# Kernel optimization log

Measured on AMD Instinct MI355X. Metric: run time of the kernel, lower is better.

Reference implementation:

```python
import jax, jax.numpy as jnp
import numpy as np

LAMDA = 0.2  # config['lamda']
T, B, NI, IL, NS, H = 24, 64, 32, 24, 256, 256  # steps, batch, n_inputs, input_len(=vec), n_stations, hidden


def setup_inputs() -> dict:
    key = jax.random.key(0)
    ks = jax.random.split(key, 24)
    VEC, DIN = IL, NI + NS
    n = lambda k, s, sc=1.0: jax.random.normal(k, s, dtype=jnp.float32) * sc
    return {
        'local_inputs': n(ks[0], (T, B, NI)),
        'global_inputs': n(ks[1], (T, B, NS)),
        'local_states': n(ks[2], (B, NI, IL)),
        'global_states': n(ks[3], (B, NS, NI, IL)),
        'distmat': n(ks[4], (B, NS)),
        'local_attn0': jax.random.uniform(ks[5], (B, NI), jnp.float32, -0.25, 0.25),
        'global_attn0': jax.random.uniform(ks[6], (B, NS), jnp.float32, -0.15, 0.15),
        # conv_local_u: 1x1 conv over [B, IL, NI, 1] -> weight [VEC, IL]
        'Wcl': n(ks[7], (VEC, IL), 0.1), 'bcl': n(ks[8], (VEC,), 0.05),
        'Wll': n(ks[9], (VEC, H), 0.05), 'bll': n(ks[10], (VEC,), 0.05),
        'vl': n(ks[11], (VEC,)),
        # conv_global_k: kernel (1, NI) over [B, IL, NS, NI] -> weight [VEC, IL, NI]
        'Wcg': n(ks[12], (VEC, IL, NI), 0.05), 'bcg': n(ks[13], (VEC,), 0.05),
        'Wlg': n(ks[14], (VEC, H), 0.05), 'blg': n(ks[15], (VEC,), 0.05),
        'vg': n(ks[16], (VEC,)),
        # LSTM cell (called with zero h0/c0 every step, as in the source)
        'Wih': n(ks[17], (4 * H, DIN), 0.05),
        'bih': n(ks[18], (4 * H,), 0.05),
        'bhh': n(ks[19], (4 * H,), 0.05),
    }


def reference(local_inputs, global_inputs, local_states, global_states, distmat,
              local_attn0, global_attn0, Wcl, bcl, Wll, bll, vl,
              Wcg, bcg, Wlg, blg, vg, Wih, bih, bhh):
    b, ni, il = local_states.shape
    ns = global_states.shape[1]
    # raw .view() reshapes as in the torch code (NOT transposes)
    lhid = local_states.reshape(b, il, ni)                 # [B, IL, NI]
    hf_l = jnp.einsum('oc,bcl->bol', Wcl, lhid) + bcl[None, :, None]   # 1x1 conv
    ghid = global_states.reshape(b, il, ns, ni)            # [B, IL, NS, NI]
    hf_g = jnp.einsum('ocj,bcsj->bos', Wcg, ghid) + bcg[None, :, None]  # (1,NI) conv

    def step(carry, xs):
        la, ga = carry
        l_inp, g_inp = xs
        x = jnp.concatenate([la * l_inp, ga * g_inp], axis=1)  # [B, NI+NS]
        gates = x @ Wih.T + bih + bhh                          # h0 = 0 -> no Whh term
        i_g, f_g, g_g, o_g = jnp.split(gates, 4, axis=1)       # torch gate order i,f,g,o
        c = jax.nn.sigmoid(i_g) * jnp.tanh(g_g)                # c0 = 0 -> forget term drops
        h = jax.nn.sigmoid(o_g) * jnp.tanh(c)
        q = c                                                  # query = LSTM state
        y_l = q @ Wll.T + bll                                  # [B, VEC]
        s_l = jnp.einsum('bold,d->bl', jnp.tanh(hf_l[:, :, :, None] + y_l[:, None, None, :]), vl)
        la_n = jax.nn.softmax(s_l, axis=1)
        y_g = q @ Wlg.T + blg
        s_g = jnp.einsum('bosd,d->bs', jnp.tanh(hf_g[:, :, :, None] + y_g[:, None, None, :]), vg)
        s_g = (1.0 - LAMDA) * s_g + LAMDA * distmat
        ga_n = jax.nn.softmax(s_g, axis=1)
        return (la_n, ga_n), (h, c, la_n, ga_n)

    _, (outs, cs, las, gas) = jax.lax.scan(step, (local_attn0, global_attn0),
                                           (local_inputs, global_inputs))
    return outs, cs[-1], las, gas
```

## Files before the change

kernel.cpp:

```cpp
#include <hip/hip_runtime.h>

#define T_     24
#define LAMDA_ 0.2f

#define OFF_CS  393216
#define OFF_LAS 409600
#define OFF_GAS 458752

__device__ __forceinline__ float clamp15(float x){ return fminf(15.f, fmaxf(-15.f, x)); }
__device__ __forceinline__ float rcp_(float x){ return __builtin_amdgcn_rcpf(x); }

__global__ __launch_bounds__(1024, 4) void spat_kernel(
    const float* __restrict__ li,  const float* __restrict__ gi,
    const float* __restrict__ ls,  const float* __restrict__ gs,
    const float* __restrict__ dist,
    const float* __restrict__ la0, const float* __restrict__ ga0,
    const float* __restrict__ Wcl, const float* __restrict__ bcl,
    const float* __restrict__ Wll, const float* __restrict__ bll, const float* __restrict__ vl,
    const float* __restrict__ Wcg, const float* __restrict__ bcg,
    const float* __restrict__ Wlg, const float* __restrict__ blg, const float* __restrict__ vg,
    const float* __restrict__ Wih, const float* __restrict__ bih, const float* __restrict__ bhh,
    float* __restrict__ out)
{
    __shared__ float Eg[6144];
    __shared__ float El[800];
    __shared__ float outb[6144];
    __shared__ float gasb[6144];
    __shared__ float lasb[768];
    __shared__ float csb[256];
    __shared__ __align__(16) union {
        float wcg[6144];
        struct {
            float sgred[1024];
            float gbuf[768];
            float xv[288];
            float cq[256];
            float slg[32];
        } p;
    } U;
    __shared__ float dstf[256];
    __shared__ float bsum[768];
    __shared__ float bcf[48];
    __shared__ __align__(16) float4 pl4[12], pg4[12];
    __shared__ float vlf[24], vgf[24], cbuf[2];

    const int b = blockIdx.x, tid = threadIdx.x;
    const int s = tid & 255, ogrp = tid >> 8;

    if (tid < 256) dstf[tid] = dist[b*256 + tid];
    if (tid < 24)  { vlf[tid] = vl[tid]; vgf[tid] = vg[tid]; }
    if (tid < 48)  bcf[tid] = (tid < 24) ? bll[tid] : blg[tid - 24];
    if (tid < 768) {
        const int wrow = tid + ((tid >= 256) ? 256 : 0);
        bsum[tid] = bih[wrow] + bhh[wrow];
    }
    if (tid == 0)  { float s1 = 0.f; for (int d = 0; d < 24; d++) s1 += vl[d]; cbuf[0] = s1; }
    if (tid == 1)  { float s1 = 0.f; for (int d = 0; d < 24; d++) s1 += vg[d]; cbuf[1] = s1; }

    float acc[6];
#pragma unroll
    for (int i = 0; i < 6; i++) acc[i] = bcg[ogrp*6 + i];

    for (int hc = 0; hc < 3; hc++) {
        for (int k = tid; k < 6144; k += 1024) {
            const int o = k >> 8, r = k & 255;
            U.wcg[k] = Wcg[o*768 + hc*256 + r];
        }
        __syncthreads();
        for (int cc = 0; cc < 8; cc++) {
            const int c = hc*8 + cc;
            const float4* gp = (const float4*)(gs + ((size_t)b*196608 + c*8192 + s*32));
#pragma unroll
            for (int h = 0; h < 2; h++) {
                float gv[16];
#pragma unroll
                for (int m = 0; m < 4; m++) {
                    const float4 g = gp[h*4 + m];
                    gv[4*m] = g.x; gv[4*m+1] = g.y; gv[4*m+2] = g.z; gv[4*m+3] = g.w;
                }
#pragma unroll
                for (int i = 0; i < 6; i++) {
                    const float4* wp = (const float4*)(U.wcg + ((ogrp*6 + i)*256 + cc*32)) + h*4;
                    float a = acc[i];
#pragma unroll
                    for (int m = 0; m < 4; m++) {
                        const float4 w = wp[m];
                        a = fmaf(w.x, gv[4*m],   a);
                        a = fmaf(w.y, gv[4*m+1], a);
                        a = fmaf(w.z, gv[4*m+2], a);
                        a = fmaf(w.w, gv[4*m+3], a);
                    }
                    acc[i] = a;
                }
            }
        }
        __syncthreads();
    }
#pragma unroll
    for (int i = 0; i < 6; i++) Eg[(ogrp*6 + i)*256 + s] = __expf(2.f*clamp15(acc[i]));

    if (tid < 768) {
        const int o = tid >> 5, l = tid & 31;
        float a = bcl[o];
        for (int c = 0; c < 24; c++)
            a = fmaf(Wcl[o*24 + c], ls[b*768 + c*32 + l], a);
        El[l*25 + o] = __expf(2.f*clamp15(a));
    }

    if (tid < 288) {
        if (tid < 32) U.p.xv[tid] = la0[b*32 + tid] * li[b*32 + tid];
        else { const int ss = tid - 32; U.p.xv[tid] = ga0[b*256 + ss] * gi[b*256 + ss]; }
    }
    __syncthreads();

    const int u8 = tid & 7, slot = tid >> 3;
    const int rbase = slot*6;
    const int lg = tid >> 5, ol = tid & 31;

    for (int t = 0; t < T_; t++) {
        float liN = 0.f;
        float giN0 = 0.f, giN1 = 0.f, giN2 = 0.f, giN3 = 0.f;
        if (t < T_ - 1) {
            if (tid < 32) liN = li[(t+1)*2048 + b*32 + tid];
            else if (tid >= 64 && tid < 128) {
                const int lane = tid - 64;
                giN0 = gi[(t+1)*16384 + b*256 + lane];
                giN1 = gi[(t+1)*16384 + b*256 + lane + 64];
                giN2 = gi[(t+1)*16384 + b*256 + lane + 128];
                giN3 = gi[(t+1)*16384 + b*256 + lane + 192];
            }
        }

        {
            const float4* xp = (const float4*)U.p.xv;
            float ar0 = 0.f, ar1 = 0.f, ar2 = 0.f, ar3 = 0.f, ar4 = 0.f, ar5 = 0.f;
#pragma unroll 1
            for (int jc = 0; jc < 3; jc++) {
                const float4 x0 = xp[jc*24 + u8];
                const float4 x1 = xp[jc*24 + 8 + u8];
                const float4 x2 = xp[jc*24 + 16 + u8];

#define KROW(kk, AR) { \
                const int row_ = rbase + (kk); \
                const int wrow_ = row_ + ((row_ >= 256) ? 256 : 0); \
                const float4* wp_ = (const float4*)(Wih + wrow_*288) + jc*24 + u8; \
                const float4 w0_ = wp_[0], w1_ = wp_[8], w2_ = wp_[16]; \
                float a_ = AR; \
                a_ = fmaf(w0_.x,x0.x,a_); a_ = fmaf(w0_.y,x0.y,a_); \
                a_ = fmaf(w0_.z,x0.z,a_); a_ = fmaf(w0_.w,x0.w,a_); \
                a_ = fmaf(w1_.x,x1.x,a_); a_ = fmaf(w1_.y,x1.y,a_); \
                a_ = fmaf(w1_.z,x1.z,a_); a_ = fmaf(w1_.w,x1.w,a_); \
                a_ = fmaf(w2_.x,x2.x,a_); a_ = fmaf(w2_.y,x2.y,a_); \
                a_ = fmaf(w2_.z,x2.z,a_); a_ = fmaf(w2_.w,x2.w,a_); \
                AR = a_; }

                KROW(0, ar0) KROW(1, ar1) KROW(2, ar2)
                __builtin_amdgcn_sched_barrier(0);
                KROW(3, ar3) KROW(4, ar4) KROW(5, ar5)
                __builtin_amdgcn_sched_barrier(0);
#undef KROW
            }
            {
                float a_;
#define RED(kk, AR) { a_ = AR; \
                a_ += __shfl_xor(a_, 1); a_ += __shfl_xor(a_, 2); a_ += __shfl_xor(a_, 4); \
                if (u8 == 0) { const int row_ = rbase + (kk); U.p.gbuf[row_] = a_ + bsum[row_]; } }
                RED(0, ar0) RED(1, ar1) RED(2, ar2) RED(3, ar3) RED(4, ar4) RED(5, ar5)
#undef RED
            }
        }
        __syncthreads();

        if (tid < 256) {
            const float ig = U.p.gbuf[tid], gg = U.p.gbuf[256 + tid], ot = U.p.gbuf[512 + tid];
            const float sig_i = rcp_(1.f + __expf(-ig));
            const float th_g  = 1.f - 2.f*rcp_(1.f + __expf(2.f*clamp15(gg)));
            const float c     = sig_i * th_g;
            const float sig_o = rcp_(1.f + __expf(-ot));
            const float th_c  = 1.f - 2.f*rcp_(1.f + __expf(2.f*c));
            const float h     = sig_o * th_c;
            U.p.cq[tid] = c;
            outb[t*256 + tid] = h;
            if (t == T_ - 1) csb[tid] = c;
        }
        __syncthreads();

        if (tid < 384) {
            const int dot = slot;
            const float* Wr = (dot < 24) ? (Wll + dot*256) : (Wlg + (dot - 24)*256);
            const float4* wp = (const float4*)Wr;
            const float4* cp = (const float4*)U.p.cq;
            float a0 = 0.f, a1 = 0.f;
#pragma unroll
            for (int j = 0; j < 8; j += 2) {
                const float4 w0 = wp[j*8 + u8],     c0 = cp[j*8 + u8];
                const float4 w1 = wp[(j+1)*8 + u8], c1 = cp[(j+1)*8 + u8];
                a0 = fmaf(w0.x,c0.x,a0); a0 = fmaf(w0.y,c0.y,a0);
                a0 = fmaf(w0.z,c0.z,a0); a0 = fmaf(w0.w,c0.w,a0);
                a1 = fmaf(w1.x,c1.x,a1); a1 = fmaf(w1.y,c1.y,a1);
                a1 = fmaf(w1.z,c1.z,a1); a1 = fmaf(w1.w,c1.w,a1);
            }
            float a = a0 + a1;
            a += __shfl_xor(a, 1); a += __shfl_xor(a, 2); a += __shfl_xor(a, 4);
            const float F  = __expf(2.f*clamp15(a + bcf[dot]));
            const float v  = (dot < 24) ? vlf[dot] : vgf[dot - 24];
            const float Fo = __shfl_xor(F, 8);
            const float vo = (dot < 24) ? vlf[dot ^ 1] : vgf[(dot ^ 1) - 24];
            if ((tid & 15) == 0) {
                const float A0 = v + vo;
                const float A1 = fmaf(v, Fo, vo * F);
                const float B1 = F + Fo;
                const float B2 = F * Fo;
                const int P = slot >> 1;
                if (P < 12) pl4[P]      = make_float4(A0, A1, B1, B2);
                else        pg4[P - 12] = make_float4(A0, A1, B1, B2);
            }
        }
        __syncthreads();

        {
            float z[6], z2[6];
#pragma unroll
            for (int i = 0; i < 6; i++) {
                z[i]  = Eg[(ogrp*6 + i)*256 + s];
                z2[i] = z[i]*z[i];
            }
            float a0 = 0.f;
#pragma unroll 4
            for (int p = 0; p < 12; p++) {
                const float4 q = pg4[p];
#pragma unroll
                for (int i = 0; i < 6; i++) {
                    const float num = fmaf(z[i],  q.y, q.x);
                    const float den = fmaf(z2[i], q.w, fmaf(z[i], q.z, 1.f));
                    a0 = fmaf(num, rcp_(den), a0);
                }
            }
            U.p.sgred[tid] = a0;
        }
        {
            float bsl = 0.f;
            if (ol < 24) {
                const float E  = El[lg*25 + ol];
                const float E2 = E*E;
#pragma unroll 4
                for (int p = 0; p < 12; p++) {
                    const float4 q = pl4[p];
                    const float num = fmaf(E,  q.y, q.x);
                    const float den = fmaf(E2, q.w, fmaf(E, q.z, 1.f));
                    bsl = fmaf(num, rcp_(den), bsl);
                }
            }
            bsl += __shfl_xor(bsl, 1);  bsl += __shfl_xor(bsl, 2);
            bsl += __shfl_xor(bsl, 4);  bsl += __shfl_xor(bsl, 8);
            bsl += __shfl_xor(bsl, 16);
            if (ol == 0) U.p.slg[lg] = bsl;
        }
        __syncthreads();

        if (tid < 32) {
            const float sv = 24.f*cbuf[0] - 2.f*U.p.slg[tid];
            float m = sv;
#pragma unroll
            for (int mk = 16; mk >= 1; mk >>= 1) m = fmaxf(m, __shfl_xor(m, mk));
            const float e = __expf(sv - m);
            float ss = e;
#pragma unroll
            for (int mk = 16; mk >= 1; mk >>= 1) ss += __shfl_xor(ss, mk);
            const float r = e * rcp_(ss);
            lasb[t*32 + tid] = r;
            if (t < T_ - 1) U.p.xv[tid] = r * liN;
        } else if (tid >= 64 && tid < 128) {
            const int lane = tid - 64;
            float vv0, vv1, vv2, vv3;
            {
                const float t0 = U.p.sgred[lane]     + U.p.sgred[256+lane]     + U.p.sgred[512+lane]     + U.p.sgred[768+lane];
                const float t1 = U.p.sgred[lane+64]  + U.p.sgred[256+lane+64]  + U.p.sgred[512+lane+64]  + U.p.sgred[768+lane+64];
                const float t2 = U.p.sgred[lane+128] + U.p.sgred[256+lane+128] + U.p.sgred[512+lane+128] + U.p.sgred[768+lane+128];
                const float t3 = U.p.sgred[lane+192] + U.p.sgred[256+lane+192] + U.p.sgred[512+lane+192] + U.p.sgred[768+lane+192];
                vv0 = (1.f-LAMDA_)*(24.f*cbuf[1] - 2.f*t0) + LAMDA_*dstf[lane];
                vv1 = (1.f-LAMDA_)*(24.f*cbuf[1] - 2.f*t1) + LAMDA_*dstf[lane+64];
                vv2 = (1.f-LAMDA_)*(24.f*cbuf[1] - 2.f*t2) + LAMDA_*dstf[lane+128];
                vv3 = (1.f-LAMDA_)*(24.f*cbuf[1] - 2.f*t3) + LAMDA_*dstf[lane+192];
            }
            float m = fmaxf(fmaxf(vv0, vv1), fmaxf(vv2, vv3));
#pragma unroll
            for (int mk = 32; mk >= 1; mk >>= 1) m = fmaxf(m, __shfl_xor(m, mk));
            const float e0 = __expf(vv0 - m), e1 = __expf(vv1 - m);
            const float e2 = __expf(vv2 - m), e3 = __expf(vv3 - m);
            float ss = (e0 + e1) + (e2 + e3);
#pragma unroll
            for (int mk = 32; mk >= 1; mk >>= 1) ss += __shfl_xor(ss, mk);
            const float inv = rcp_(ss);
            const float r0 = e0*inv, r1 = e1*inv, r2 = e2*inv, r3 = e3*inv;
            float* gb = gasb + t*256;
            gb[lane] = r0; gb[lane+64] = r1; gb[lane+128] = r2; gb[lane+192] = r3;
            if (t < T_ - 1) {
                U.p.xv[32+lane]     = r0 * giN0;
                U.p.xv[32+lane+64]  = r1 * giN1;
                U.p.xv[32+lane+128] = r2 * giN2;
                U.p.xv[32+lane+192] = r3 * giN3;
            }
        }
        __syncthreads();
    }

    for (int k = tid; k < 6144; k += 1024) {
        const int tt = k >> 8, ii = k & 255;
        out[tt*16384 + b*256 + ii]           = outb[k];
        out[OFF_GAS + tt*16384 + b*256 + ii] = gasb[k];
    }
    if (tid < 768) out[OFF_LAS + (tid >> 5)*2048 + b*32 + (tid & 31)] = lasb[tid];
    if (tid < 256) out[OFF_CS + b*256 + tid] = csb[tid];
}

extern "C" void kernel_launch(void* const* d_in, const int* in_sizes, int n_in,
                              void* d_out, int out_size, void* d_ws, size_t ws_size,
                              hipStream_t stream)
{
    const float* li   = (const float*)d_in[0];
    const float* gi   = (const float*)d_in[1];
    const float* ls   = (const float*)d_in[2];
    const float* gs   = (const float*)d_in[3];
    const float* dist = (const float*)d_in[4];
    const float* la0  = (const float*)d_in[5];
    const float* ga0  = (const float*)d_in[6];
    const float* Wcl  = (const float*)d_in[7];
    const float* bcl  = (const float*)d_in[8];
    const float* Wll  = (const float*)d_in[9];
    const float* bll  = (const float*)d_in[10];
    const float* vl   = (const float*)d_in[11];
    const float* Wcg  = (const float*)d_in[12];
    const float* bcg  = (const float*)d_in[13];
    const float* Wlg  = (const float*)d_in[14];
    const float* blg  = (const float*)d_in[15];
    const float* vg   = (const float*)d_in[16];
    const float* Wih  = (const float*)d_in[17];
    const float* bih  = (const float*)d_in[18];
    const float* bhh  = (const float*)d_in[19];

    spat_kernel<<<64, 1024, 0, stream>>>(li, gi, ls, gs, dist, la0, ga0,
                                         Wcl, bcl, Wll, bll, vl,
                                         Wcg, bcg, Wlg, blg, vg,
                                         Wih, bih, bhh, (float*)d_out);
}
```

Baseline: 506.2 us.

## Replace per-element tanh attention sums with per-step cubic-interpolated lookup tables

Result: slower. 535.0 us (+5.7%).

```diff
diff --git a/kernel.cpp b/kernel.cpp
--- a/kernel.cpp
+++ b/kernel.cpp
@@ -6,6 +6,10 @@
 #define OFF_CS  393216
 #define OFF_LAS 409600
 #define OFF_GAS 458752
+
+#define TBL_N   1024
+#define TBL_H   (32.0f/1023.0f)
+#define TBL_IH  (1023.0f/32.0f)
 
 __device__ __forceinline__ float clamp15(float x){ return fminf(15.f, fmaxf(-15.f, x)); }
 __device__ __forceinline__ float rcp_(float x){ return __builtin_amdgcn_rcpf(x); }
@@ -22,8 +26,6 @@
     const float* __restrict__ Wih, const float* __restrict__ bih, const float* __restrict__ bhh,
     float* __restrict__ out)
 {
-    __shared__ float Eg[6144];
-    __shared__ float El[800];
     __shared__ float outb[6144];
     __shared__ float gasb[6144];
     __shared__ float lasb[768];
@@ -38,10 +40,12 @@
             float slg[32];
         } p;
     } U;
+    __shared__ float gt[TBL_N];
+    __shared__ float lt[TBL_N];
+    __shared__ __align__(8) float2 ygp[24], ylp[24];
     __shared__ float dstf[256];
     __shared__ float bsum[768];
     __shared__ float bcf[48];
-    __shared__ __align__(16) float4 pl4[12], pg4[12];
     __shared__ float vlf[24], vgf[24], cbuf[2];
 
     const int b = blockIdx.x, tid = threadIdx.x;
@@ -96,15 +100,34 @@
         }
         __syncthreads();
     }
-#pragma unroll
-    for (int i = 0; i < 6; i++) Eg[(ogrp*6 + i)*256 + s] = __expf(2.f*clamp15(acc[i]));
-
-    if (tid < 768) {
-        const int o = tid >> 5, l = tid & 31;
-        float a = bcl[o];
+
+    const int lg = tid >> 5, ol = tid & 31;
+
+    float al_a = 0.f;
+    if (ol < 24) {
+        float a = bcl[ol];
         for (int c = 0; c < 24; c++)
-            a = fmaf(Wcl[o*24 + c], ls[b*768 + c*32 + l], a);
-        El[l*25 + o] = __expf(2.f*clamp15(a));
+            a = fmaf(Wcl[ol*24 + c], ls[b*768 + c*32 + lg], a);
+        al_a = a;
+    }
+
+    int   mg[6];  float4 wg[6];
+    int   mlx;    float4 wlx;
+    {
+#define MKW(AVAL, MM, WW) { \
+        const float t_  = (clamp15(AVAL) + 16.f) * TBL_IH; \
+        const float jf_ = floorf(t_); \
+        const float f_  = t_ - jf_; \
+        MM = (int)jf_ - 1; \
+        const float fp_ = f_ + 1.f, fm_ = f_ - 1.f, f2_ = f_ - 2.f; \
+        WW.x = -f_*fm_*f2_*(1.f/6.f); \
+        WW.y =  fp_*fm_*f2_*0.5f; \
+        WW.z = -fp_*f_*f2_*0.5f; \
+        WW.w =  fp_*f_*fm_*(1.f/6.f); }
+#pragma unroll
+        for (int i = 0; i < 6; i++) MKW(acc[i], mg[i], wg[i])
+        MKW(al_a, mlx, wlx)
+#undef MKW
     }
 
     if (tid < 288) {
@@ -115,7 +138,6 @@
 
     const int u8 = tid & 7, slot = tid >> 3;
     const int rbase = slot*6;
-    const int lg = tid >> 5, ol = tid & 31;
 
     for (int t = 0; t < T_; t++) {
         float liN = 0.f;
@@ -202,54 +224,50 @@
             }
             float a = a0 + a1;
             a += __shfl_xor(a, 1); a += __shfl_xor(a, 2); a += __shfl_xor(a, 4);
-            const float F  = __expf(2.f*clamp15(a + bcf[dot]));
-            const float v  = (dot < 24) ? vlf[dot] : vgf[dot - 24];
-            const float Fo = __shfl_xor(F, 8);
-            const float vo = (dot < 24) ? vlf[dot ^ 1] : vgf[(dot ^ 1) - 24];
-            if ((tid & 15) == 0) {
-                const float A0 = v + vo;
-                const float A1 = fmaf(v, Fo, vo * F);
-                const float B1 = F + Fo;
-                const float B2 = F * Fo;
-                const int P = slot >> 1;
-                if (P < 12) pl4[P]      = make_float4(A0, A1, B1, B2);
-                else        pg4[P - 12] = make_float4(A0, A1, B1, B2);
+            if (u8 == 0) {
+                const float y = a + bcf[dot];
+                if (dot < 24) ylp[dot]      = make_float2(2.f*y, vlf[dot]);
+                else          ygp[dot - 24] = make_float2(2.f*y, vgf[dot - 24]);
             }
         }
         __syncthreads();
 
         {
-            float z[6], z2[6];
+            const float ak2 = 2.f*(-16.f + (float)tid * TBL_H);
+            float sg_ = 0.f, sl_ = 0.f;
+#pragma unroll 4
+            for (int d = 0; d < 24; d++) {
+                const float2 pg = ygp[d];
+                const float2 pl = ylp[d];
+                sg_ = fmaf(pg.y, rcp_(1.f + __expf(ak2 + pg.x)), sg_);
+                sl_ = fmaf(pl.y, rcp_(1.f + __expf(ak2 + pl.x)), sl_);
+            }
+            gt[tid] = cbuf[1] - 2.f*sg_;
+            lt[tid] = cbuf[0] - 2.f*sl_;
+        }
+        __syncthreads();
+
+        {
+            float a0 = 0.f;
 #pragma unroll
             for (int i = 0; i < 6; i++) {
-                z[i]  = Eg[(ogrp*6 + i)*256 + s];
-                z2[i] = z[i]*z[i];
-            }
-            float a0 = 0.f;
-#pragma unroll 4
-            for (int p = 0; p < 12; p++) {
-                const float4 q = pg4[p];
-#pragma unroll
-                for (int i = 0; i < 6; i++) {
-                    const float num = fmaf(z[i],  q.y, q.x);
-                    const float den = fmaf(z2[i], q.w, fmaf(z[i], q.z, 1.f));
-                    a0 = fmaf(num, rcp_(den), a0);
-                }
+                const float* p_ = gt + mg[i];
+                float v_ = wg[i].x * p_[0];
+                v_ = fmaf(wg[i].y, p_[1], v_);
+                v_ = fmaf(wg[i].z, p_[2], v_);
+                v_ = fmaf(wg[i].w, p_[3], v_);
+                a0 += v_;
             }
             U.p.sgred[tid] = a0;
         }
         {
             float bsl = 0.f;
             if (ol < 24) {
-                const float E  = El[lg*25 + ol];
-                const float E2 = E*E;
-#pragma unroll 4
-                for (int p = 0; p < 12; p++) {
-                    const float4 q = pl4[p];
-                    const float num = fmaf(E,  q.y, q.x);
-                    const float den = fmaf(E2, q.w, fmaf(E, q.z, 1.f));
-                    bsl = fmaf(num, rcp_(den), bsl);
-                }
+                const float* p_ = lt + mlx;
+                bsl = wlx.x * p_[0];
+                bsl = fmaf(wlx.y, p_[1], bsl);
+                bsl = fmaf(wlx.z, p_[2], bsl);
+                bsl = fmaf(wlx.w, p_[3], bsl);
             }
             bsl += __shfl_xor(bsl, 1);  bsl += __shfl_xor(bsl, 2);
             bsl += __shfl_xor(bsl, 4);  bsl += __shfl_xor(bsl, 8);
@@ -259,7 +277,7 @@
         __syncthreads();
 
         if (tid < 32) {
-            const float sv = 24.f*cbuf[0] - 2.f*U.p.slg[tid];
+            const float sv = U.p.slg[tid];
             float m = sv;
 #pragma unroll
             for (int mk = 16; mk >= 1; mk >>= 1) m = fmaxf(m, __shfl_xor(m, mk));
@@ -278,10 +296,10 @@
                 const float t1 = U.p.sgred[lane+64]  + U.p.sgred[256+lane+64]  + U.p.sgred[512+lane+64]  + U.p.sgred[768+lane+64];
                 const float t2 = U.p.sgred[lane+128] + U.p.sgred[256+lane+128] + U.p.sgred[512+lane+128] + U.p.sgred[768+lane+128];
                 const float t3 = U.p.sgred[lane+192] + U.p.sgred[256+lane+192] + U.p.sgred[512+lane+192] + U.p.sgred[768+lane+192];
-                vv0 = (1.f-LAMDA_)*(24.f*cbuf[1] - 2.f*t0) + LAMDA_*dstf[lane];
-                vv1 = (1.f-LAMDA_)*(24.f*cbuf[1] - 2.f*t1) + LAMDA_*dstf[lane+64];
-                vv2 = (1.f-LAMDA_)*(24.f*cbuf[1] - 2.f*t2) + LAMDA_*dstf[lane+128];
-                vv3 = (1.f-LAMDA_)*(24.f*cbuf[1] - 2.f*t3) + LAMDA_*dstf[lane+192];
+                vv0 = (1.f-LAMDA_)*t0 + LAMDA_*dstf[lane];
+                vv1 = (1.f-LAMDA_)*t1 + LAMDA_*dstf[lane+64];
+                vv2 = (1.f-LAMDA_)*t2 + LAMDA_*dstf[lane+128];
+                vv3 = (1.f-LAMDA_)*t3 + LAMDA_*dstf[lane+192];
             }
             float m = fmaxf(fmaxf(vv0, vv1), fmaxf(vv2, vv3));
 #pragma unroll
```

## Split each batch row across four cooperating blocks with register-resident LSTM weights

Applied to the files above, without the earlier changes.

Result: slower. 716.0 us (+41.5%).

```diff
diff --git a/kernel.cpp b/kernel.cpp
--- a/kernel.cpp
+++ b/kernel.cpp
@@ -20,42 +20,74 @@
     const float* __restrict__ Wcg, const float* __restrict__ bcg,
     const float* __restrict__ Wlg, const float* __restrict__ blg, const float* __restrict__ vg,
     const float* __restrict__ Wih, const float* __restrict__ bih, const float* __restrict__ bhh,
-    float* __restrict__ out)
+    float* __restrict__ ws, float* __restrict__ out)
 {
     __shared__ float Eg[6144];
     __shared__ float El[800];
-    __shared__ float outb[6144];
-    __shared__ float gasb[6144];
-    __shared__ float lasb[768];
-    __shared__ float csb[256];
+    __shared__ float outb[1536];
+    __shared__ float gasb[1536];
+    __shared__ float lasb[192];
+    __shared__ float csb[64];
     __shared__ __align__(16) union {
         float wcg[6144];
         struct {
             float sgred[1024];
-            float gbuf[768];
+            float cqf[256];
             float xv[288];
-            float cq[256];
             float slg[32];
         } p;
     } U;
     __shared__ float dstf[256];
-    __shared__ float bsum[768];
     __shared__ float bcf[48];
     __shared__ __align__(16) float4 pl4[12], pg4[12];
     __shared__ float vlf[24], vgf[24], cbuf[2];
-
-    const int b = blockIdx.x, tid = threadIdx.x;
+    __shared__ float ldspad[5632];
+
+    const int bid = blockIdx.x;
+    const int b = bid >> 2, K = bid & 3;
+    const int tid = threadIdx.x;
     const int s = tid & 255, ogrp = tid >> 8;
+
+    float* wsb = ws + (size_t)b * 1024;
+    int*   wst = (int*)(wsb + 512);
+
+    if (__builtin_expect((int)blockIdx.x == 0x7fffffff, 0)) {
+        ldspad[tid] = bcg[0];
+        out[0] = ldspad[tid ^ 1];
+    }
 
     if (tid < 256) dstf[tid] = dist[b*256 + tid];
     if (tid < 24)  { vlf[tid] = vl[tid]; vgf[tid] = vg[tid]; }
     if (tid < 48)  bcf[tid] = (tid < 24) ? bll[tid] : blg[tid - 24];
-    if (tid < 768) {
-        const int wrow = tid + ((tid >= 256) ? 256 : 0);
-        bsum[tid] = bih[wrow] + bhh[wrow];
-    }
     if (tid == 0)  { float s1 = 0.f; for (int d = 0; d < 24; d++) s1 += vl[d]; cbuf[0] = s1; }
     if (tid == 1)  { float s1 = 0.f; for (int d = 0; d < 24; d++) s1 += vg[d]; cbuf[1] = s1; }
+
+    const int slot = tid >> 3, u8 = tid & 7;
+    const int pairu = slot >> 1;
+    const bool isEven = (slot & 1) == 0;
+    const int u_glob = K*64 + pairu;
+    const float bsI = bih[u_glob]     + bhh[u_glob];
+    const float bsG = bih[512+u_glob] + bhh[512+u_glob];
+    const float bsO = bih[768+u_glob] + bhh[768+u_glob];
+
+    float4 wA[9], wB[9];
+    {
+        const float4* W4 = (const float4*)Wih;
+        const int cb = u8*9;
+        if (isEven) {
+#pragma unroll
+            for (int m = 0; m < 9; m++) {
+                wA[m] = W4[(size_t)u_glob*72 + cb + m];
+                wB[m] = W4[(size_t)(512+u_glob)*72 + cb + m];
+            }
+        } else {
+#pragma unroll
+            for (int m = 0; m < 9; m++) {
+                wA[m] = W4[(size_t)(768+u_glob)*72 + cb + m];
+                wB[m] = make_float4(0.f,0.f,0.f,0.f);
+            }
+        }
+    }
 
     float acc[6];
 #pragma unroll
@@ -113,8 +145,6 @@
     }
     __syncthreads();
 
-    const int u8 = tid & 7, slot = tid >> 3;
-    const int rbase = slot*6;
     const int lg = tid >> 5, ol = tid & 31;
 
     for (int t = 0; t < T_; t++) {
@@ -132,88 +162,83 @@
         }
 
         {
-            const float4* xp = (const float4*)U.p.xv;
-            float ar0 = 0.f, ar1 = 0.f, ar2 = 0.f, ar3 = 0.f, ar4 = 0.f, ar5 = 0.f;
-#pragma unroll 1
-            for (int jc = 0; jc < 3; jc++) {
-                const float4 x0 = xp[jc*24 + u8];
-                const float4 x1 = xp[jc*24 + 8 + u8];
-                const float4 x2 = xp[jc*24 + 16 + u8];
-
-#define KROW(kk, AR) { \
-                const int row_ = rbase + (kk); \
-                const int wrow_ = row_ + ((row_ >= 256) ? 256 : 0); \
-                const float4* wp_ = (const float4*)(Wih + wrow_*288) + jc*24 + u8; \
-                const float4 w0_ = wp_[0], w1_ = wp_[8], w2_ = wp_[16]; \
-                float a_ = AR; \
-                a_ = fmaf(w0_.x,x0.x,a_); a_ = fmaf(w0_.y,x0.y,a_); \
-                a_ = fmaf(w0_.z,x0.z,a_); a_ = fmaf(w0_.w,x0.w,a_); \
-                a_ = fmaf(w1_.x,x1.x,a_); a_ = fmaf(w1_.y,x1.y,a_); \
-                a_ = fmaf(w1_.z,x1.z,a_); a_ = fmaf(w1_.w,x1.w,a_); \
-                a_ = fmaf(w2_.x,x2.x,a_); a_ = fmaf(w2_.y,x2.y,a_); \
-                a_ = fmaf(w2_.z,x2.z,a_); a_ = fmaf(w2_.w,x2.w,a_); \
-                AR = a_; }
-
-                KROW(0, ar0) KROW(1, ar1) KROW(2, ar2)
-                __builtin_amdgcn_sched_barrier(0);
-                KROW(3, ar3) KROW(4, ar4) KROW(5, ar5)
-                __builtin_amdgcn_sched_barrier(0);
-#undef KROW
-            }
-            {
-                float a_;
-#define RED(kk, AR) { a_ = AR; \
-                a_ += __shfl_xor(a_, 1); a_ += __shfl_xor(a_, 2); a_ += __shfl_xor(a_, 4); \
-                if (u8 == 0) { const int row_ = rbase + (kk); U.p.gbuf[row_] = a_ + bsum[row_]; } }
-                RED(0, ar0) RED(1, ar1) RED(2, ar2) RED(3, ar3) RED(4, ar4) RED(5, ar5)
-#undef RED
-            }
-        }
-        __syncthreads();
-
-        if (tid < 256) {
-            const float ig = U.p.gbuf[tid], gg = U.p.gbuf[256 + tid], ot = U.p.gbuf[512 + tid];
-            const float sig_i = rcp_(1.f + __expf(-ig));
-            const float th_g  = 1.f - 2.f*rcp_(1.f + __expf(2.f*clamp15(gg)));
-            const float c     = sig_i * th_g;
-            const float sig_o = rcp_(1.f + __expf(-ot));
-            const float th_c  = 1.f - 2.f*rcp_(1.f + __expf(2.f*c));
-            const float h     = sig_o * th_c;
-            U.p.cq[tid] = c;
-            outb[t*256 + tid] = h;
-            if (t == T_ - 1) csb[tid] = c;
-        }
-        __syncthreads();
-
-        if (tid < 384) {
-            const int dot = slot;
+            const float4* xp4 = (const float4*)U.p.xv;
+            float aA = 0.f, aB = 0.f;
+#pragma unroll
+            for (int m = 0; m < 9; m++) {
+                const float4 x4 = xp4[u8*9 + m];
+                aA = fmaf(wA[m].x, x4.x, aA); aA = fmaf(wA[m].y, x4.y, aA);
+                aA = fmaf(wA[m].z, x4.z, aA); aA = fmaf(wA[m].w, x4.w, aA);
+                if (isEven) {
+                    aB = fmaf(wB[m].x, x4.x, aB); aB = fmaf(wB[m].y, x4.y, aB);
+                    aB = fmaf(wB[m].z, x4.z, aB); aB = fmaf(wB[m].w, x4.w, aB);
+                }
+            }
+            aA += __shfl_xor(aA, 1); aA += __shfl_xor(aA, 2); aA += __shfl_xor(aA, 4);
+            aB += __shfl_xor(aB, 1); aB += __shfl_xor(aB, 2); aB += __shfl_xor(aB, 4);
+            const float aO = __shfl_down(aA, 8);
+            if ((tid & 15) == 0) {
+                const float ig = aA + bsI, gg = aB + bsG, ot = aO + bsO;
+                const float sig_i = rcp_(1.f + __expf(-ig));
+                const float th_g  = 1.f - 2.f*rcp_(1.f + __expf(2.f*clamp15(gg)));
+                const float c     = sig_i * th_g;
+                const float sig_o = rcp_(1.f + __expf(-ot));
+                const float th_c  = 1.f - 2.f*rcp_(1.f + __expf(2.f*c));
+                const float h     = sig_o * th_c;
+                U.p.cqf[u_glob] = c;
+                outb[t*64 + pairu] = h;
+                if (t == T_ - 1) csb[pairu] = c;
+                wsb[(t&1)*256 + K*64 + pairu] = c;
+            }
+        }
+        __syncthreads();
+
+        if (tid == 0)
+            __hip_atomic_store(&wst[(t&1)*4 + K], t+1,
+                               __ATOMIC_RELEASE, __HIP_MEMORY_SCOPE_AGENT);
+        if (tid < 192) {
+            const int pp = tid >> 6;
+            const int P  = pp + (pp >= K ? 1 : 0);
+            const int j  = tid & 63;
+            while (__hip_atomic_load(&wst[(t&1)*4 + P],
+                                     __ATOMIC_ACQUIRE, __HIP_MEMORY_SCOPE_AGENT) != t+1)
+                __builtin_amdgcn_s_sleep(1);
+            U.p.cqf[P*64 + j] =
+                __hip_atomic_load(&wsb[(t&1)*256 + P*64 + j],
+                                  __ATOMIC_RELAXED, __HIP_MEMORY_SCOPE_AGENT);
+        }
+        __syncthreads();
+
+        if (tid < 768) {
+            const int dot = tid >> 4, l16 = tid & 15;
             const float* Wr = (dot < 24) ? (Wll + dot*256) : (Wlg + (dot - 24)*256);
-            const float4* wp = (const float4*)Wr;
-            const float4* cp = (const float4*)U.p.cq;
+            const float4* wp = (const float4*)Wr + l16*4;
+            const float4* cp = (const float4*)U.p.cqf + l16*4;
             float a0 = 0.f, a1 = 0.f;
 #pragma unroll
-            for (int j = 0; j < 8; j += 2) {
-                const float4 w0 = wp[j*8 + u8],     c0 = cp[j*8 + u8];
-                const float4 w1 = wp[(j+1)*8 + u8], c1 = cp[(j+1)*8 + u8];
+            for (int m = 0; m < 4; m += 2) {
+                const float4 w0 = wp[m],   c0 = cp[m];
+                const float4 w1 = wp[m+1], c1 = cp[m+1];
                 a0 = fmaf(w0.x,c0.x,a0); a0 = fmaf(w0.y,c0.y,a0);
                 a0 = fmaf(w0.z,c0.z,a0); a0 = fmaf(w0.w,c0.w,a0);
                 a1 = fmaf(w1.x,c1.x,a1); a1 = fmaf(w1.y,c1.y,a1);
                 a1 = fmaf(w1.z,c1.z,a1); a1 = fmaf(w1.w,c1.w,a1);
             }
             float a = a0 + a1;
-            a += __shfl_xor(a, 1); a += __shfl_xor(a, 2); a += __shfl_xor(a, 4);
+            a += __shfl_xor(a, 1); a += __shfl_xor(a, 2);
+            a += __shfl_xor(a, 4); a += __shfl_xor(a, 8);
             const float F  = __expf(2.f*clamp15(a + bcf[dot]));
             const float v  = (dot < 24) ? vlf[dot] : vgf[dot - 24];
-            const float Fo = __shfl_xor(F, 8);
+            const float Fo = __shfl_xor(F, 16);
             const float vo = (dot < 24) ? vlf[dot ^ 1] : vgf[(dot ^ 1) - 24];
-            if ((tid & 15) == 0) {
+            if ((tid & 31) == 0) {
                 const float A0 = v + vo;
                 const float A1 = fmaf(v, Fo, vo * F);
                 const float B1 = F + Fo;
                 const float B2 = F * Fo;
-                const int P = slot >> 1;
-                if (P < 12) pl4[P]      = make_float4(A0, A1, B1, B2);
-                else        pg4[P - 12] = make_float4(A0, A1, B1, B2);
+                const int P2 = dot >> 1;
+                if (P2 < 12) pl4[P2]      = make_float4(A0, A1, B1, B2);
+                else         pg4[P2 - 12] = make_float4(A0, A1, B1, B2);
             }
         }
         __syncthreads();
@@ -268,7 +293,7 @@
 #pragma unroll
             for (int mk = 16; mk >= 1; mk >>= 1) ss += __shfl_xor(ss, mk);
             const float r = e * rcp_(ss);
-            lasb[t*32 + tid] = r;
+            if ((tid >> 3) == K) lasb[t*8 + (tid & 7)] = r;
             if (t < T_ - 1) U.p.xv[tid] = r * liN;
         } else if (tid >= 64 && tid < 128) {
             const int lane = tid - 64;
@@ -293,8 +318,8 @@
             for (int mk = 32; mk >= 1; mk >>= 1) ss += __shfl_xor(ss, mk);
             const float inv = rcp_(ss);
             const float r0 = e0*inv, r1 = e1*inv, r2 = e2*inv, r3 = e3*inv;
-            float* gb = gasb + t*256;
-            gb[lane] = r0; gb[lane+64] = r1; gb[lane+128] = r2; gb[lane+192] = r3;
+            const float rK = (K == 0) ? r0 : (K == 1) ? r1 : (K == 2) ? r2 : r3;
+            gasb[t*64 + lane] = rK;
             if (t < T_ - 1) {
                 U.p.xv[32+lane]     = r0 * giN0;
                 U.p.xv[32+lane+64]  = r1 * giN1;
@@ -305,13 +330,16 @@
         __syncthreads();
     }
 
-    for (int k = tid; k < 6144; k += 1024) {
-        const int tt = k >> 8, ii = k & 255;
-        out[tt*16384 + b*256 + ii]           = outb[k];
-        out[OFF_GAS + tt*16384 + b*256 + ii] = gasb[k];
-    }
-    if (tid < 768) out[OFF_LAS + (tid >> 5)*2048 + b*32 + (tid & 31)] = lasb[tid];
-    if (tid < 256) out[OFF_CS + b*256 + tid] = csb[tid];
+    for (int k = tid; k < 1536; k += 1024) {
+        const int tt = k >> 6, j = k & 63;
+        out[tt*16384 + b*256 + K*64 + j]           = outb[k];
+        out[OFF_GAS + tt*16384 + b*256 + K*64 + j] = gasb[k];
+    }
+    if (tid < 192) {
+        const int tt = tid >> 3, j = tid & 7;
+        out[OFF_LAS + tt*2048 + b*32 + K*8 + j] = lasb[tid];
+    }
+    if (tid < 64) out[OFF_CS + b*256 + K*64 + tid] = csb[tid];
 }
 
 extern "C" void kernel_launch(void* const* d_in, const int* in_sizes, int n_in,
@@ -339,8 +367,11 @@
     const float* bih  = (const float*)d_in[18];
     const float* bhh  = (const float*)d_in[19];
 
-    spat_kernel<<<64, 1024, 0, stream>>>(li, gi, ls, gs, dist, la0, ga0,
-                                         Wcl, bcl, Wll, bll, vl,
-                                         Wcg, bcg, Wlg, blg, vg,
-                                         Wih, bih, bhh, (float*)d_out);
+    hipMemsetAsync(d_ws, 0, 64 * 1024 * sizeof(float), stream);
+
+    spat_kernel<<<256, 1024, 0, stream>>>(li, gi, ls, gs, dist, la0, ga0,
+                                          Wcl, bcl, Wll, bll, vl,
+                                          Wcg, bcg, Wlg, blg, vg,
+                                          Wih, bih, bhh,
+                                          (float*)d_ws, (float*)d_out);
 }
```

## Fuse LSTM gate reduction with activation and pack attention math into v2f FMAs

Applied to the files above, without the earlier changes.

Result: faster. 484.3 us (-4.3%).

```diff
diff --git a/kernel.cpp b/kernel.cpp
--- a/kernel.cpp
+++ b/kernel.cpp
@@ -9,6 +9,9 @@
 
 __device__ __forceinline__ float clamp15(float x){ return fminf(15.f, fmaxf(-15.f, x)); }
 __device__ __forceinline__ float rcp_(float x){ return __builtin_amdgcn_rcpf(x); }
+
+typedef float v2f __attribute__((ext_vector_type(2)));
+#define PKFMA(a,b,c) __builtin_elementwise_fma((a),(b),(c))
 
 __global__ __launch_bounds__(1024, 4) void spat_kernel(
     const float* __restrict__ li,  const float* __restrict__ gi,
@@ -28,11 +31,11 @@
     __shared__ float gasb[6144];
     __shared__ float lasb[768];
     __shared__ float csb[256];
+    __shared__ float slred[800];
     __shared__ __align__(16) union {
         float wcg[6144];
         struct {
             float sgred[1024];
-            float gbuf[768];
             float xv[288];
             float cq[256];
             float slg[32];
@@ -114,8 +117,7 @@
     __syncthreads();
 
     const int u8 = tid & 7, slot = tid >> 3;
-    const int rbase = slot*6;
-    const int lg = tid >> 5, ol = tid & 31;
+    const int u0 = slot*2;
 
     for (int t = 0; t < T_; t++) {
         float liN = 0.f;
@@ -140,10 +142,8 @@
                 const float4 x1 = xp[jc*24 + 8 + u8];
                 const float4 x2 = xp[jc*24 + 16 + u8];
 
-#define KROW(kk, AR) { \
-                const int row_ = rbase + (kk); \
-                const int wrow_ = row_ + ((row_ >= 256) ? 256 : 0); \
-                const float4* wp_ = (const float4*)(Wih + wrow_*288) + jc*24 + u8; \
+#define KROW(WROW, AR) { \
+                const float4* wp_ = (const float4*)(Wih + (size_t)(WROW)*288) + jc*24 + u8; \
                 const float4 w0_ = wp_[0], w1_ = wp_[8], w2_ = wp_[16]; \
                 float a_ = AR; \
                 a_ = fmaf(w0_.x,x0.x,a_); a_ = fmaf(w0_.y,x0.y,a_); \
@@ -154,112 +154,122 @@
                 a_ = fmaf(w2_.z,x2.z,a_); a_ = fmaf(w2_.w,x2.w,a_); \
                 AR = a_; }
 
-                KROW(0, ar0) KROW(1, ar1) KROW(2, ar2)
+                KROW(u0,       ar0) KROW(512 + u0, ar1) KROW(768 + u0, ar2)
                 __builtin_amdgcn_sched_barrier(0);
-                KROW(3, ar3) KROW(4, ar4) KROW(5, ar5)
+                KROW(u0 + 1,   ar3) KROW(513 + u0, ar4) KROW(769 + u0, ar5)
                 __builtin_amdgcn_sched_barrier(0);
 #undef KROW
             }
-            {
-                float a_;
-#define RED(kk, AR) { a_ = AR; \
-                a_ += __shfl_xor(a_, 1); a_ += __shfl_xor(a_, 2); a_ += __shfl_xor(a_, 4); \
-                if (u8 == 0) { const int row_ = rbase + (kk); U.p.gbuf[row_] = a_ + bsum[row_]; } }
-                RED(0, ar0) RED(1, ar1) RED(2, ar2) RED(3, ar3) RED(4, ar4) RED(5, ar5)
-#undef RED
-            }
-        }
-        __syncthreads();
-
-        if (tid < 256) {
-            const float ig = U.p.gbuf[tid], gg = U.p.gbuf[256 + tid], ot = U.p.gbuf[512 + tid];
-            const float sig_i = rcp_(1.f + __expf(-ig));
-            const float th_g  = 1.f - 2.f*rcp_(1.f + __expf(2.f*clamp15(gg)));
-            const float c     = sig_i * th_g;
-            const float sig_o = rcp_(1.f + __expf(-ot));
-            const float th_c  = 1.f - 2.f*rcp_(1.f + __expf(2.f*c));
-            const float h     = sig_o * th_c;
-            U.p.cq[tid] = c;
-            outb[t*256 + tid] = h;
-            if (t == T_ - 1) csb[tid] = c;
-        }
-        __syncthreads();
-
-        if (tid < 384) {
-            const int dot = slot;
+            ar0 += __shfl_xor(ar0, 1); ar0 += __shfl_xor(ar0, 2); ar0 += __shfl_xor(ar0, 4);
+            ar1 += __shfl_xor(ar1, 1); ar1 += __shfl_xor(ar1, 2); ar1 += __shfl_xor(ar1, 4);
+            ar2 += __shfl_xor(ar2, 1); ar2 += __shfl_xor(ar2, 2); ar2 += __shfl_xor(ar2, 4);
+            ar3 += __shfl_xor(ar3, 1); ar3 += __shfl_xor(ar3, 2); ar3 += __shfl_xor(ar3, 4);
+            ar4 += __shfl_xor(ar4, 1); ar4 += __shfl_xor(ar4, 2); ar4 += __shfl_xor(ar4, 4);
+            ar5 += __shfl_xor(ar5, 1); ar5 += __shfl_xor(ar5, 2); ar5 += __shfl_xor(ar5, 4);
+            if (u8 < 2) {
+                const int uu = u0 + u8;
+                const float ig = (u8 ? ar3 : ar0) + bsum[uu];
+                const float gg = (u8 ? ar4 : ar1) + bsum[256 + uu];
+                const float ot = (u8 ? ar5 : ar2) + bsum[512 + uu];
+                const float sig_i = rcp_(1.f + __expf(-ig));
+                const float th_g  = 1.f - 2.f*rcp_(1.f + __expf(2.f*clamp15(gg)));
+                const float c     = sig_i * th_g;
+                const float sig_o = rcp_(1.f + __expf(-ot));
+                const float th_c  = 1.f - 2.f*rcp_(1.f + __expf(2.f*c));
+                const float h     = sig_o * th_c;
+                U.p.cq[uu] = c;
+                outb[t*256 + uu] = h;
+                if (t == T_ - 1) csb[uu] = c;
+            }
+        }
+        __syncthreads();
+
+        if (tid < 768) {
+            const int dot = tid >> 4, l16 = tid & 15;
             const float* Wr = (dot < 24) ? (Wll + dot*256) : (Wlg + (dot - 24)*256);
-            const float4* wp = (const float4*)Wr;
-            const float4* cp = (const float4*)U.p.cq;
+            const float4* wp = (const float4*)Wr + l16*4;
+            const float4* cp = (const float4*)U.p.cq + l16*4;
             float a0 = 0.f, a1 = 0.f;
 #pragma unroll
-            for (int j = 0; j < 8; j += 2) {
-                const float4 w0 = wp[j*8 + u8],     c0 = cp[j*8 + u8];
-                const float4 w1 = wp[(j+1)*8 + u8], c1 = cp[(j+1)*8 + u8];
+            for (int m = 0; m < 4; m += 2) {
+                const float4 w0 = wp[m],   c0 = cp[m];
+                const float4 w1 = wp[m+1], c1 = cp[m+1];
                 a0 = fmaf(w0.x,c0.x,a0); a0 = fmaf(w0.y,c0.y,a0);
                 a0 = fmaf(w0.z,c0.z,a0); a0 = fmaf(w0.w,c0.w,a0);
                 a1 = fmaf(w1.x,c1.x,a1); a1 = fmaf(w1.y,c1.y,a1);
                 a1 = fmaf(w1.z,c1.z,a1); a1 = fmaf(w1.w,c1.w,a1);
             }
             float a = a0 + a1;
-            a += __shfl_xor(a, 1); a += __shfl_xor(a, 2); a += __shfl_xor(a, 4);
+            a += __shfl_xor(a, 1); a += __shfl_xor(a, 2);
+            a += __shfl_xor(a, 4); a += __shfl_xor(a, 8);
             const float F  = __expf(2.f*clamp15(a + bcf[dot]));
             const float v  = (dot < 24) ? vlf[dot] : vgf[dot - 24];
-            const float Fo = __shfl_xor(F, 8);
+            const float Fo = __shfl_xor(F, 16);
             const float vo = (dot < 24) ? vlf[dot ^ 1] : vgf[(dot ^ 1) - 24];
-            if ((tid & 15) == 0) {
+            if ((tid & 31) == 0) {
                 const float A0 = v + vo;
                 const float A1 = fmaf(v, Fo, vo * F);
                 const float B1 = F + Fo;
                 const float B2 = F * Fo;
-                const int P = slot >> 1;
-                if (P < 12) pl4[P]      = make_float4(A0, A1, B1, B2);
-                else        pg4[P - 12] = make_float4(A0, A1, B1, B2);
+                const int P2 = dot >> 1;
+                if (P2 < 12) pl4[P2]      = make_float4(A0, A1, B1, B2);
+                else         pg4[P2 - 12] = make_float4(A0, A1, B1, B2);
             }
         }
         __syncthreads();
 
         {
-            float z[6], z2[6];
-#pragma unroll
-            for (int i = 0; i < 6; i++) {
-                z[i]  = Eg[(ogrp*6 + i)*256 + s];
-                z2[i] = z[i]*z[i];
-            }
-            float a0 = 0.f;
+            float z[6];
+#pragma unroll
+            for (int i = 0; i < 6; i++) z[i] = Eg[(ogrp*6 + i)*256 + s];
+            const v2f zv0 = {z[0], z[1]}, zv1 = {z[2], z[3]}, zv2 = {z[4], z[5]};
+            const v2f z2v0 = zv0*zv0, z2v1 = zv1*zv1, z2v2 = zv2*zv2;
+            const v2f one2 = {1.f, 1.f};
+            v2f acc2 = {0.f, 0.f};
 #pragma unroll 4
             for (int p = 0; p < 12; p++) {
                 const float4 q = pg4[p];
-#pragma unroll
-                for (int i = 0; i < 6; i++) {
-                    const float num = fmaf(z[i],  q.y, q.x);
-                    const float den = fmaf(z2[i], q.w, fmaf(z[i], q.z, 1.f));
-                    a0 = fmaf(num, rcp_(den), a0);
-                }
-            }
-            U.p.sgred[tid] = a0;
-        }
-        {
-            float bsl = 0.f;
-            if (ol < 24) {
-                const float E  = El[lg*25 + ol];
-                const float E2 = E*E;
+                const v2f qx = {q.x, q.x}, qy = {q.y, q.y};
+                const v2f qz = {q.z, q.z}, qw = {q.w, q.w};
+                const v2f n0 = PKFMA(zv0, qy, qx);
+                const v2f n1 = PKFMA(zv1, qy, qx);
+                const v2f n2 = PKFMA(zv2, qy, qx);
+                const v2f d0 = PKFMA(z2v0, qw, PKFMA(zv0, qz, one2));
+                const v2f d1 = PKFMA(z2v1, qw, PKFMA(zv1, qz, one2));
+                const v2f d2 = PKFMA(z2v2, qw, PKFMA(zv2, qz, one2));
+                const v2f r0 = {rcp_(d0.x), rcp_(d0.y)};
+                const v2f r1 = {rcp_(d1.x), rcp_(d1.y)};
+                const v2f r2 = {rcp_(d2.x), rcp_(d2.y)};
+                acc2 = PKFMA(n0, r0, acc2);
+                acc2 = PKFMA(n1, r1, acc2);
+                acc2 = PKFMA(n2, r2, acc2);
+            }
+            U.p.sgred[tid] = acc2.x + acc2.y;
+        }
+        if (tid < 768) {
+            const int l = tid / 24, o = tid - l*24;
+            const float E  = El[l*25 + o];
+            const float E2 = E*E;
+            float b0 = 0.f, b1 = 0.f;
 #pragma unroll 4
-                for (int p = 0; p < 12; p++) {
-                    const float4 q = pl4[p];
-                    const float num = fmaf(E,  q.y, q.x);
-                    const float den = fmaf(E2, q.w, fmaf(E, q.z, 1.f));
-                    bsl = fmaf(num, rcp_(den), bsl);
-                }
-            }
-            bsl += __shfl_xor(bsl, 1);  bsl += __shfl_xor(bsl, 2);
-            bsl += __shfl_xor(bsl, 4);  bsl += __shfl_xor(bsl, 8);
-            bsl += __shfl_xor(bsl, 16);
-            if (ol == 0) U.p.slg[lg] = bsl;
+            for (int p = 0; p < 12; p += 2) {
+                const float4 q0 = pl4[p], q1 = pl4[p+1];
+                const float n0 = fmaf(E, q0.y, q0.x);
+                const float d0 = fmaf(E2, q0.w, fmaf(E, q0.z, 1.f));
+                const float n1 = fmaf(E, q1.y, q1.x);
+                const float d1 = fmaf(E2, q1.w, fmaf(E, q1.z, 1.f));
+                b0 = fmaf(n0, rcp_(d0), b0);
+                b1 = fmaf(n1, rcp_(d1), b1);
+            }
+            slred[l*25 + o] = b0 + b1;
         }
         __syncthreads();
 
         if (tid < 32) {
-            const float sv = 24.f*cbuf[0] - 2.f*U.p.slg[tid];
+            float tot = 0.f;
+#pragma unroll
+            for (int o2 = 0; o2 < 24; o2++) tot += slred[tid*25 + o2];
+            const float sv = 24.f*cbuf[0] - 2.f*tot;
             float m = sv;
 #pragma unroll
             for (int mk = 16; mk >= 1; mk >>= 1) m = fmaxf(m, __shfl_xor(m, mk));
```
